# Kernel optimization log

Hardware: AMD Instinct MI355X
Metric: run time of the kernel (lower is better)

## Reference

```python
import jax, jax.numpy as jnp
import numpy as np

NEG_SLOPE = 0.2  # leaky_relu negative slope (alpha)

def _glorot(key, shape):
    fan_in, fan_out = shape[0], shape[-1]
    lim = jnp.sqrt(6.0 / (fan_in + fan_out))
    return jax.random.uniform(key, shape, jnp.float32, -lim, lim)

def setup_inputs() -> dict:
    key = jax.random.key(0)
    ks = jax.random.split(key, 10)
    N, E, F_IN, HID, HEADS, NCLASS = 50000, 800000, 512, 32, 8, 32
    x = jax.random.normal(ks[0], (N, F_IN), jnp.float32)
    edge_index = jax.random.randint(ks[1], (2, E), 0, N, jnp.int64)
    # layer 1: heads=8, out per head = 32, concat -> 256
    W1 = _glorot(ks[2], (F_IN, HEADS * HID))
    att_src1 = _glorot(ks[3], (HEADS, HID))
    att_dst1 = _glorot(ks[4], (HEADS, HID))
    b1 = jnp.zeros((HEADS * HID,), jnp.float32)
    # layer 2: heads=1, out = nclass
    W2 = _glorot(ks[5], (HEADS * HID, NCLASS))
    att_src2 = _glorot(ks[6], (1, NCLASS))
    att_dst2 = _glorot(ks[7], (1, NCLASS))
    b2 = jnp.zeros((NCLASS,), jnp.float32)
    return {"x": x, "edge_index": edge_index, "W1": W1, "att_src1": att_src1,
            "att_dst1": att_dst1, "b1": b1, "W2": W2, "att_src2": att_src2,
            "att_dst2": att_dst2, "b2": b2}

def gat_conv(x, src, dst, W, a_src, a_dst, bias, num_nodes):
    """PyG GATConv (eval mode, self loops already appended to src/dst)."""
    H, C = a_src.shape
    h = (x @ W).reshape(num_nodes, H, C)                 # [N,H,C]
    score_src = jnp.einsum('nhc,hc->nh', h, a_src)       # [N,H]
    score_dst = jnp.einsum('nhc,hc->nh', h, a_dst)       # [N,H]
    e = jax.nn.leaky_relu(score_src[src] + score_dst[dst], NEG_SLOPE)  # [E,H]
    m = jax.ops.segment_max(e, dst, num_segments=num_nodes)           # [N,H]
    w = jnp.exp(e - m[dst])
    denom = jax.ops.segment_sum(w, dst, num_segments=num_nodes)       # [N,H]
    alpha = w / (denom[dst] + 1e-16)                                  # [E,H]
    out = jax.ops.segment_sum(alpha[:, :, None] * h[src], dst,
                              num_segments=num_nodes)                 # [N,H,C]
    return out.reshape(num_nodes, H * C) + bias

def reference(x, edge_index, W1, att_src1, att_dst1, b1, W2, att_src2, att_dst2, b2):
    N = x.shape[0]
    loops = jnp.arange(N, dtype=edge_index.dtype)
    src = jnp.concatenate([edge_index[0], loops])  # PyG add_self_loops=True
    dst = jnp.concatenate([edge_index[1], loops])
    h = jax.nn.elu(gat_conv(x, src, dst, W1, att_src1, att_dst1, b1, N))
    out = gat_conv(h, src, dst, W2, att_src2, att_dst2, b2, N)
    return out + 1e-06
```

## Files before the change

kernel.cpp:

```cpp
#include <hip/hip_runtime.h>
#include <math.h>

#define N_NODES 50000
#define N_EDGES 800000
#define E2 (N_EDGES + N_NODES)
#define F_IN 512
#define HEADS 8
#define HID 32
#define HC 256
#define NCLASS 32
#define NEG_SLOPE 0.2f

typedef unsigned int uint;
typedef unsigned short ushort;
typedef __attribute__((ext_vector_type(8))) short bf16x8;
typedef __attribute__((ext_vector_type(4))) float f32x4;

#define GLOBAL_LOAD_LDS16(g, l) \
    __builtin_amdgcn_global_load_lds((const __attribute__((address_space(1))) void*)(g), \
                                     (__attribute__((address_space(3))) void*)(l), 16, 0, 0)

__device__ inline uint bf16_rne_bits(float f) {
    uint u = __float_as_uint(f);
    return (u + 0x7fffu + ((u >> 16) & 1u)) >> 16;
}
__device__ inline float bf2f(ushort u) { return __uint_as_float(((uint)u) << 16); }

__global__ void split_w1t_kernel(const float* __restrict__ W1,
                                 ushort* __restrict__ hi, ushort* __restrict__ lo) {
    int t = blockIdx.x * 256 + threadIdx.x;
    int n = t >> 9, k = t & 511;
    float f = W1[k * 256 + n];
    uint h = bf16_rne_bits(f);
    float r = f - __uint_as_float(h << 16);
    hi[t] = (ushort)h;
    lo[t] = (ushort)bf16_rne_bits(r);
}

__global__ void split_w2t_kernel(const float* __restrict__ W2,
                                 ushort* __restrict__ hi, ushort* __restrict__ lo) {
    int t = blockIdx.x * 256 + threadIdx.x;
    int n = t >> 8, k = t & 255;
    float f = W2[k * 32 + n];
    uint h = bf16_rne_bits(f);
    float r = f - __uint_as_float(h << 16);
    hi[t] = (ushort)h;
    lo[t] = (ushort)bf16_rne_bits(r);
}

__global__ void __launch_bounds__(256) gemm1_mfma_kernel(const uint* __restrict__ xp,
        const ushort* __restrict__ bhi, const ushort* __restrict__ blo,
        const float* __restrict__ as1, const float* __restrict__ ad1,
        ushort* __restrict__ C, float* __restrict__ ssrc, float* __restrict__ sdst, int M) {
    __shared__ uint   As[128 * 32];
    __shared__ ushort Bh[128 * 32];
    __shared__ ushort Bl[128 * 32];
    const int tid = threadIdx.x, lane = tid & 63, wave = tid >> 6;
    const int bm = blockIdx.x * 128, bn = blockIdx.y * 128;

    const uint* agp[4]; const uint* alp[4];
    #pragma unroll
    for (int s = 0; s < 4; ++s) {
        int t = wave * 4 + s;
        int p = t * 64 + lane;
        int row = p >> 3, cs = p & 7;
        int c = cs ^ (row & 7);
        int grow = bm + row; if (grow > M - 1) grow = M - 1;
        agp[s] = xp + ((size_t)grow * 512 + c * 4);
        alp[s] = &As[t * 256];
    }
    const ushort* bhgp[2]; const ushort* blgp[2]; const ushort* bhlp[2]; const ushort* bllp[2];
    #pragma unroll
    for (int s = 0; s < 2; ++s) {
        int t = wave * 2 + s;
        int p = t * 64 + lane;
        int row = p >> 2, qs = p & 3;
        int q = qs ^ ((row >> 1) & 3);
        size_t go = (size_t)(bn + row) * 512 + q * 8;
        bhgp[s] = bhi + go; blgp[s] = blo + go;
        bhlp[s] = &Bh[t * 512]; bllp[s] = &Bl[t * 512];
    }

    f32x4 acc[4][4] = {};
    const int wm = (wave >> 1) * 64, wn = (wave & 1) * 64;
    const int fm = lane & 15, quad = lane >> 4;

    for (int kk = 0; kk < 16; ++kk) {
        #pragma unroll
        for (int s = 0; s < 4; ++s) GLOBAL_LOAD_LDS16(agp[s], alp[s]);
        #pragma unroll
        for (int s = 0; s < 2; ++s) {
            GLOBAL_LOAD_LDS16(bhgp[s], bhlp[s]);
            GLOBAL_LOAD_LDS16(blgp[s], bllp[s]);
        }
        #pragma unroll
        for (int s = 0; s < 4; ++s) agp[s] += 32;
        #pragma unroll
        for (int s = 0; s < 2; ++s) { bhgp[s] += 32; blgp[s] += 32; }
        __syncthreads();

        bf16x8 ah[4], al[4], bh[4], bl[4];
        #pragma unroll
        for (int i = 0; i < 4; ++i) {
            int row = wm + i * 16 + fm;
            int sw = row & 7;
            uint4 c0 = *(const uint4*)&As[row * 32 + (((2 * quad)     ^ sw) * 4)];
            uint4 c1 = *(const uint4*)&As[row * 32 + (((2 * quad + 1) ^ sw) * 4)];
            union { uint u[4]; bf16x8 v; } H, L;
            H.u[0] = __builtin_amdgcn_perm(c0.y, c0.x, 0x07060302u);
            H.u[1] = __builtin_amdgcn_perm(c0.w, c0.z, 0x07060302u);
            H.u[2] = __builtin_amdgcn_perm(c1.y, c1.x, 0x07060302u);
            H.u[3] = __builtin_amdgcn_perm(c1.w, c1.z, 0x07060302u);
            uint r0 = __float_as_uint(__uint_as_float(c0.x) - __uint_as_float(c0.x & 0xffff0000u));
            uint r1 = __float_as_uint(__uint_as_float(c0.y) - __uint_as_float(c0.y & 0xffff0000u));
            uint r2 = __float_as_uint(__uint_as_float(c0.z) - __uint_as_float(c0.z & 0xffff0000u));
            uint r3 = __float_as_uint(__uint_as_float(c0.w) - __uint_as_float(c0.w & 0xffff0000u));
            uint r4 = __float_as_uint(__uint_as_float(c1.x) - __uint_as_float(c1.x & 0xffff0000u));
            uint r5 = __float_as_uint(__uint_as_float(c1.y) - __uint_as_float(c1.y & 0xffff0000u));
            uint r6 = __float_as_uint(__uint_as_float(c1.z) - __uint_as_float(c1.z & 0xffff0000u));
            uint r7 = __float_as_uint(__uint_as_float(c1.w) - __uint_as_float(c1.w & 0xffff0000u));
            L.u[0] = __builtin_amdgcn_perm(r1, r0, 0x07060302u);
            L.u[1] = __builtin_amdgcn_perm(r3, r2, 0x07060302u);
            L.u[2] = __builtin_amdgcn_perm(r5, r4, 0x07060302u);
            L.u[3] = __builtin_amdgcn_perm(r7, r6, 0x07060302u);
            ah[i] = H.v; al[i] = L.v;
        }
        #pragma unroll
        for (int j = 0; j < 4; ++j) {
            int row = wn + j * 16 + fm;
            int qs = quad ^ ((row >> 1) & 3);
            bh[j] = *(const bf16x8*)&Bh[row * 32 + qs * 8];
            bl[j] = *(const bf16x8*)&Bl[row * 32 + qs * 8];
        }
        #pragma unroll
        for (int i = 0; i < 4; ++i)
            #pragma unroll
            for (int j = 0; j < 4; ++j) {
                acc[i][j] = __builtin_amdgcn_mfma_f32_16x16x32_bf16(ah[i], bh[j], acc[i][j], 0, 0, 0);
                acc[i][j] = __builtin_amdgcn_mfma_f32_16x16x32_bf16(ah[i], bl[j], acc[i][j], 0, 0, 0);
                acc[i][j] = __builtin_amdgcn_mfma_f32_16x16x32_bf16(al[i], bh[j], acc[i][j], 0, 0, 0);
            }
        __syncthreads();
    }

    #pragma unroll
    for (int i = 0; i < 4; ++i) {
        int rb = bm + wm + i * 16 + quad * 4;
        #pragma unroll
        for (int j = 0; j < 4; ++j) {
            int col = bn + wn + j * 16 + fm;
            #pragma unroll
            for (int r = 0; r < 4; ++r) {
                int row = rb + r;
                if (row < M) C[(size_t)row * 256 + col] = (ushort)bf16_rne_bits(acc[i][j][r]);
            }
        }
    }

    const int head0 = (bn + wn) >> 5;
    const float asA0 = as1[head0 * 32 + fm],      asA1 = as1[head0 * 32 + 16 + fm];
    const float asB0 = as1[head0 * 32 + 32 + fm], asB1 = as1[head0 * 32 + 48 + fm];
    const float adA0 = ad1[head0 * 32 + fm],      adA1 = ad1[head0 * 32 + 16 + fm];
    const float adB0 = ad1[head0 * 32 + 32 + fm], adB1 = ad1[head0 * 32 + 48 + fm];
    #pragma unroll
    for (int i = 0; i < 4; ++i) {
        #pragma unroll
        for (int r = 0; r < 4; ++r) {
            int row = bm + wm + i * 16 + quad * 4 + r;
            float s1A = acc[i][0][r] * asA0 + acc[i][1][r] * asA1;
            float s1B = acc[i][2][r] * asB0 + acc[i][3][r] * asB1;
            float s2A = acc[i][0][r] * adA0 + acc[i][1][r] * adA1;
            float s2B = acc[i][2][r] * adB0 + acc[i][3][r] * adB1;
            #pragma unroll
            for (int off = 1; off < 16; off <<= 1) {
                s1A += __shfl_xor(s1A, off);
                s1B += __shfl_xor(s1B, off);
                s2A += __shfl_xor(s2A, off);
                s2B += __shfl_xor(s2B, off);
            }
            if (fm == 0 && row < M) {
                ssrc[(size_t)row * 8 + head0]     = s1A;
                ssrc[(size_t)row * 8 + head0 + 1] = s1B;
                sdst[(size_t)row * 8 + head0]     = s2A;
                sdst[(size_t)row * 8 + head0 + 1] = s2B;
            }
        }
    }
}

__global__ void __launch_bounds__(256) gemm2_mfma_kernel(const ushort* __restrict__ A,
        const ushort* __restrict__ bh_g, const ushort* __restrict__ bl_g,
        const float* __restrict__ as2, const float* __restrict__ ad2,
        ushort* __restrict__ C, float* __restrict__ ssrc, float* __restrict__ sdst, int M) {
    __shared__ ushort As[128 * 32];
    const int tid = threadIdx.x, lane = tid & 63, wave = tid >> 6;
    const int bm = blockIdx.x * 128;
    const int fm = lane & 15, quad = lane >> 4;
    const int wrow = wave * 32;

    const ushort* agp[2]; const ushort* alp[2];
    #pragma unroll
    for (int s = 0; s < 2; ++s) {
        int t = wave * 2 + s;
        int p = t * 64 + lane;
        int row = p >> 2, qs = p & 3;
        int q = qs ^ ((row >> 1) & 3);
        int gr = bm + row; if (gr > M - 1) gr = M - 1;
        agp[s] = A + (size_t)gr * 256 + q * 8;
        alp[s] = &As[t * 512];
    }

    f32x4 acc[2][2] = {};
    for (int kk = 0; kk < 8; ++kk) {
        GLOBAL_LOAD_LDS16(agp[0], alp[0]);
        GLOBAL_LOAD_LDS16(agp[1], alp[1]);
        agp[0] += 32; agp[1] += 32;
        __syncthreads();
        bf16x8 a[2], bh[2], bl[2];
        #pragma unroll
        for (int i = 0; i < 2; ++i) {
            int row = wrow + i * 16 + fm;
            int q = quad ^ ((row >> 1) & 3);
            a[i] = *(const bf16x8*)&As[row * 32 + q * 8];
        }
        #pragma unroll
        for (int j = 0; j < 2; ++j) {
            size_t off = (size_t)(j * 16 + fm) * 256 + kk * 32 + quad * 8;
            bh[j] = *(const bf16x8*)(bh_g + off);
            bl[j] = *(const bf16x8*)(bl_g + off);
        }
        #pragma unroll
        for (int i = 0; i < 2; ++i)
            #pragma unroll
            for (int j = 0; j < 2; ++j) {
                acc[i][j] = __builtin_amdgcn_mfma_f32_16x16x32_bf16(a[i], bh[j], acc[i][j], 0, 0, 0);
                acc[i][j] = __builtin_amdgcn_mfma_f32_16x16x32_bf16(a[i], bl[j], acc[i][j], 0, 0, 0);
            }
        __syncthreads();
    }

    float a0 = as2[fm], a1 = as2[16 + fm];
    float d0 = ad2[fm], d1 = ad2[16 + fm];
    #pragma unroll
    for (int i = 0; i < 2; ++i) {
        #pragma unroll
        for (int r = 0; r < 4; ++r) {
            int rg = bm + wrow + i * 16 + quad * 4 + r;
            float v0 = acc[i][0][r], v1 = acc[i][1][r];
            float s1 = v0 * a0 + v1 * a1;
            float s2 = v0 * d0 + v1 * d1;
            #pragma unroll
            for (int off = 1; off < 16; off <<= 1) {
                s1 += __shfl_xor(s1, off);
                s2 += __shfl_xor(s2, off);
            }
            if (rg < M) {
                C[(size_t)rg * 32 + fm]      = (ushort)bf16_rne_bits(v0);
                C[(size_t)rg * 32 + 16 + fm] = (ushort)bf16_rne_bits(v1);
                if (fm == 0) { ssrc[rg] = s1; sdst[rg] = s2; }
            }
        }
    }
}

__global__ void count_deg(const int* __restrict__ ei, int* __restrict__ deg) {
    int e = blockIdx.x * blockDim.x + threadIdx.x;
    if (e >= E2) return;
    int dst = (e < N_EDGES) ? ei[N_EDGES + e] : (e - N_EDGES);
    atomicAdd(&deg[dst], 1);
}

#define SCAN_B 256
#define SCAN_NB ((N_NODES + SCAN_B - 1) / SCAN_B)

__global__ void scan1_kernel(const int* __restrict__ deg, int* __restrict__ rowstart,
                             int* __restrict__ blocksum) {
    __shared__ int sm[SCAN_B];
    int t = threadIdx.x, i = blockIdx.x * SCAN_B + t;
    int v = (i < N_NODES) ? deg[i] : 0;
    sm[t] = v; __syncthreads();
    int x = v;
    for (int off = 1; off < SCAN_B; off <<= 1) {
        int y = (t >= off) ? sm[t - off] : 0; __syncthreads();
        x += y; sm[t] = x; __syncthreads();
    }
    if (i <= N_NODES) rowstart[i] = x - v;
    if (t == SCAN_B - 1) blocksum[blockIdx.x] = x;
}

__global__ void scan2_kernel(const int* __restrict__ blocksum, int* __restrict__ blockoff) {
    __shared__ int sm[256];
    int t = threadIdx.x;
    int v = (t < SCAN_NB) ? blocksum[t] : 0;
    sm[t] = v; __syncthreads();
    int x = v;
    for (int off = 1; off < 256; off <<= 1) {
        int y = (t >= off) ? sm[t - off] : 0; __syncthreads();
        x += y; sm[t] = x; __syncthreads();
    }
    if (t < SCAN_NB) blockoff[t] = x - v;
}

__global__ void fill_csr(const int* __restrict__ ei, const int* __restrict__ rowstart,
                         const int* __restrict__ blockoff,
                         int* __restrict__ cursor, int* __restrict__ csr_src) {
    int e = blockIdx.x * blockDim.x + threadIdx.x;
    if (e >= E2) return;
    int src, dst;
    if (e < N_EDGES) { src = ei[e]; dst = ei[N_EDGES + e]; }
    else             { src = e - N_EDGES; dst = src; }
    int p = atomicAdd(&cursor[dst], 1);
    csr_src[rowstart[dst] + blockoff[dst >> 8] + p] = src;
}

__global__ void __launch_bounds__(256) agg1_wave_kernel(const ushort* __restrict__ h,
        const float* __restrict__ ssrc, const float* __restrict__ sdst,
        const int* __restrict__ rowstart, const int* __restrict__ blockoff,
        const int* __restrict__ csr_src,
        const float* __restrict__ bias, ushort* __restrict__ out) {
    const int wid = (blockIdx.x * blockDim.x + threadIdx.x) >> 6;
    if (wid >= N_NODES) return;
    const int lane = threadIdx.x & 63;
    const int hg = lane >> 3;
    const int hl = lane & 7;
    const int n = wid;
    const int beg = rowstart[n] + blockoff[n >> 8];
    const int end = rowstart[n + 1] + blockoff[(n + 1) >> 8];
    const float sdst_n = sdst[(size_t)n * HEADS + hg];

    float4 acc = make_float4(0.f, 0.f, 0.f, 0.f);
    float sw = 0.f;
    const ushort* hc = h + lane * 4;
    const int base = hg << 3;
    for (int e = beg; e < end; e += 16) {
        int ee0 = e + hl, ee1 = e + 8 + hl;
        int ei0 = ee0 < end ? ee0 : end - 1;
        int ei1 = ee1 < end ? ee1 : end - 1;
        int s0 = csr_src[ei0];
        int s1 = csr_src[ei1];
        float c0 = ssrc[(size_t)s0 * HEADS + hg] + sdst_n;
        float c1 = ssrc[(size_t)s1 * HEADS + hg] + sdst_n;
        c0 = c0 > 0.f ? c0 : NEG_SLOPE * c0;
        c1 = c1 > 0.f ? c1 : NEG_SLOPE * c1;
        float w0 = (ee0 < end) ? __expf(c0) : 0.f;
        float w1 = (ee1 < end) ? __expf(c1) : 0.f;
        float wj[16]; int sj[16];
        #pragma unroll
        for (int j = 0; j < 8; ++j) {
            wj[j]     = __shfl(w0, base + j);
            sj[j]     = __shfl(s0, base + j);
            wj[8 + j] = __shfl(w1, base + j);
            sj[8 + j] = __shfl(s1, base + j);
        }
        ushort4 v[16];
        #pragma unroll
        for (int j = 0; j < 16; ++j) v[j] = *(const ushort4*)(hc + (size_t)sj[j] * HC);
        #pragma unroll
        for (int j = 0; j < 16; ++j) {
            acc.x += wj[j] * bf2f(v[j].x);
            acc.y += wj[j] * bf2f(v[j].y);
            acc.z += wj[j] * bf2f(v[j].z);
            acc.w += wj[j] * bf2f(v[j].w);
            sw += wj[j];
        }
    }
    float inv = 1.f / (sw + 1e-16f);
    float4 bv = *(const float4*)(bias + lane * 4);
    float4 o;
    o.x = acc.x * inv + bv.x; o.y = acc.y * inv + bv.y;
    o.z = acc.z * inv + bv.z; o.w = acc.w * inv + bv.w;
    o.x = o.x > 0.f ? o.x : expm1f(o.x);
    o.y = o.y > 0.f ? o.y : expm1f(o.y);
    o.z = o.z > 0.f ? o.z : expm1f(o.z);
    o.w = o.w > 0.f ? o.w : expm1f(o.w);
    ushort4 ob;
    ob.x = (ushort)bf16_rne_bits(o.x);
    ob.y = (ushort)bf16_rne_bits(o.y);
    ob.z = (ushort)bf16_rne_bits(o.z);
    ob.w = (ushort)bf16_rne_bits(o.w);
    *(ushort4*)(out + (size_t)n * HC + lane * 4) = ob;
}

__global__ void __launch_bounds__(256) agg2_kernel(const ushort* __restrict__ h2,
        const float* __restrict__ ssrc, const float* __restrict__ sdst,
        const int* __restrict__ rowstart, const int* __restrict__ blockoff,
        const int* __restrict__ csr_src,
        const float* __restrict__ bias, float* __restrict__ out) {
    const int n = blockIdx.x * 4 + (threadIdx.x >> 6);
    if (n >= N_NODES) return;
    const int beg = rowstart[n] + blockoff[n >> 8];
    const int end = rowstart[n + 1] + blockoff[(n + 1) >> 8];
    const int t = threadIdx.x & 63;
    const float sdst_n = sdst[n];

    const int slot = t >> 4, cp = t & 15;
    float a0 = 0.f, a1 = 0.f, sw = 0.f;
    for (int e = beg + slot; e < end; e += 4) {
        int src = csr_src[e];
        float sc = ssrc[src] + sdst_n;
        sc = sc > 0.f ? sc : NEG_SLOPE * sc;
        float w = __expf(sc);
        uint v = *(const uint*)(h2 + (size_t)src * NCLASS + cp * 2);
        a0 += w * __uint_as_float(v << 16);
        a1 += w * __uint_as_float(v & 0xffff0000u);
        sw += w;
    }
    a0 += __shfl_down(a0, 32); a1 += __shfl_down(a1, 32); sw += __shfl_down(sw, 32);
    a0 += __shfl_down(a0, 16); a1 += __shfl_down(a1, 16); sw += __shfl_down(sw, 16);
    if (t < 16) {
        float inv = 1.f / (sw + 1e-16f);
        float2 o;
        o.x = a0 * inv + bias[cp * 2]     + 1e-6f;
        o.y = a1 * inv + bias[cp * 2 + 1] + 1e-6f;
        *(float2*)(out + (size_t)n * NCLASS + cp * 2) = o;
    }
}

extern "C" void kernel_launch(void* const* d_in, const int* in_sizes, int n_in,
                              void* d_out, int out_size, void* d_ws, size_t ws_size,
                              hipStream_t stream) {
    const float* x        = (const float*)d_in[0];
    const int*   ei       = (const int*)  d_in[1];
    const float* W1       = (const float*)d_in[2];
    const float* att_src1 = (const float*)d_in[3];
    const float* att_dst1 = (const float*)d_in[4];
    const float* b1       = (const float*)d_in[5];
    const float* W2       = (const float*)d_in[6];
    const float* att_src2 = (const float*)d_in[7];
    const float* att_dst2 = (const float*)d_in[8];
    const float* b2       = (const float*)d_in[9];
    float* out = (float*)d_out;

    ushort* w1t_hi = (ushort*)d_ws;
    ushort* w1t_lo = w1t_hi + 256 * 512;
    ushort* w2t_hi = w1t_lo + 256 * 512;
    ushort* w2t_lo = w2t_hi + 32 * 256;
    ushort* h1b    = w2t_lo + 32 * 256;
    ushort* h2b    = h1b + (size_t)N_NODES * HC;
    ushort* out1b  = h2b + (size_t)N_NODES * NCLASS;
    float* ssrc1 = (float*)(out1b + (size_t)N_NODES * HC);
    float* sdst1 = ssrc1 + (size_t)N_NODES * HEADS;
    float* ssrc2 = sdst1 + (size_t)N_NODES * HEADS;
    float* sdst2 = ssrc2 + N_NODES;
    int* rowstart = (int*)(sdst2 + N_NODES);
    int* deg      = rowstart + N_NODES + 1;
    int* cursor   = deg + N_NODES;
    int* csr_src  = cursor + N_NODES;
    int* blocksum = csr_src + E2;
    int* blockoff = blocksum + SCAN_NB;

    hipMemsetAsync(deg, 0, 2 * N_NODES * sizeof(int), stream);
    int eb = (E2 + 255) / 256;
    count_deg<<<eb, 256, 0, stream>>>(ei, deg);
    scan1_kernel<<<SCAN_NB, SCAN_B, 0, stream>>>(deg, rowstart, blocksum);
    scan2_kernel<<<1, 256, 0, stream>>>(blocksum, blockoff);
    fill_csr<<<eb, 256, 0, stream>>>(ei, rowstart, blockoff, cursor, csr_src);

    split_w1t_kernel<<<(256 * 512) / 256, 256, 0, stream>>>(W1, w1t_hi, w1t_lo);
    split_w2t_kernel<<<(32 * 256) / 256, 256, 0, stream>>>(W2, w2t_hi, w2t_lo);

    {
        dim3 grid((N_NODES + 127) / 128, HC / 128);
        gemm1_mfma_kernel<<<grid, 256, 0, stream>>>((const uint*)x, w1t_hi, w1t_lo,
                att_src1, att_dst1, h1b, ssrc1, sdst1, N_NODES);
    }
    agg1_wave_kernel<<<(N_NODES + 3) / 4, 256, 0, stream>>>(h1b, ssrc1, sdst1, rowstart, blockoff, csr_src, b1, out1b);

    gemm2_mfma_kernel<<<(N_NODES + 127) / 128, 256, 0, stream>>>(out1b, w2t_hi, w2t_lo,
            att_src2, att_dst2, h2b, ssrc2, sdst2, N_NODES);
    agg2_kernel<<<(N_NODES + 3) / 4, 256, 0, stream>>>(h2b, ssrc2, sdst2, rowstart, blockoff, csr_src, b2, out);
}
```

Baseline: 410.2 us.

## Load GEMM A operands directly to registers and fuse prep kernels

Merges the W1/W2 bf16 hi/lo split kernels and the degree-count kernel into one launch. In gemm1 the fp32 A tile is now read straight from global memory into registers in MFMA fragment layout instead of being staged through swizzled LDS. In gemm2 the A operand is likewise read directly from global memory and the per-iteration barriers are dropped. This aims to cut launch overhead, LDS traffic and synchronisation, at the cost of less coalesced global reads and the loss of LDS staging for A.

```diff
diff --git a/kernel.cpp b/kernel.cpp
--- a/kernel.cpp
+++ b/kernel.cpp
@@ -26,49 +26,51 @@
 }
 __device__ inline float bf2f(ushort u) { return __uint_as_float(((uint)u) << 16); }
 
-__global__ void split_w1t_kernel(const float* __restrict__ W1,
-                                 ushort* __restrict__ hi, ushort* __restrict__ lo) {
-    int t = blockIdx.x * 256 + threadIdx.x;
-    int n = t >> 9, k = t & 511;
-    float f = W1[k * 256 + n];
-    uint h = bf16_rne_bits(f);
-    float r = f - __uint_as_float(h << 16);
-    hi[t] = (ushort)h;
-    lo[t] = (ushort)bf16_rne_bits(r);
-}
-
-__global__ void split_w2t_kernel(const float* __restrict__ W2,
-                                 ushort* __restrict__ hi, ushort* __restrict__ lo) {
-    int t = blockIdx.x * 256 + threadIdx.x;
-    int n = t >> 8, k = t & 255;
-    float f = W2[k * 32 + n];
-    uint h = bf16_rne_bits(f);
-    float r = f - __uint_as_float(h << 16);
-    hi[t] = (ushort)h;
-    lo[t] = (ushort)bf16_rne_bits(r);
+#define W1_BLOCKS 512
+#define W2_BLOCKS 32
+#define DEG_BLOCKS ((E2 + 255) / 256)
+
+__global__ void __launch_bounds__(256) prep_kernel(const float* __restrict__ W1,
+        ushort* __restrict__ w1hi, ushort* __restrict__ w1lo,
+        const float* __restrict__ W2, ushort* __restrict__ w2hi, ushort* __restrict__ w2lo,
+        const int* __restrict__ ei, int* __restrict__ deg) {
+    int b = blockIdx.x;
+    if (b < W1_BLOCKS) {
+        int t = b * 256 + threadIdx.x;
+        int n = t >> 9, k = t & 511;
+        float f = W1[k * 256 + n];
+        uint h = bf16_rne_bits(f);
+        float r = f - __uint_as_float(h << 16);
+        w1hi[t] = (ushort)h;
+        w1lo[t] = (ushort)bf16_rne_bits(r);
+    } else if (b < W1_BLOCKS + W2_BLOCKS) {
+        int t = (b - W1_BLOCKS) * 256 + threadIdx.x;
+        int n = t >> 8, k = t & 255;
+        float f = W2[k * 32 + n];
+        uint h = bf16_rne_bits(f);
+        float r = f - __uint_as_float(h << 16);
+        w2hi[t] = (ushort)h;
+        w2lo[t] = (ushort)bf16_rne_bits(r);
+    } else {
+        int e = (b - W1_BLOCKS - W2_BLOCKS) * 256 + threadIdx.x;
+        if (e < E2) {
+            int dst = (e < N_EDGES) ? ei[N_EDGES + e] : (e - N_EDGES);
+            atomicAdd(&deg[dst], 1);
+        }
+    }
 }
 
 __global__ void __launch_bounds__(256) gemm1_mfma_kernel(const uint* __restrict__ xp,
         const ushort* __restrict__ bhi, const ushort* __restrict__ blo,
         const float* __restrict__ as1, const float* __restrict__ ad1,
         ushort* __restrict__ C, float* __restrict__ ssrc, float* __restrict__ sdst, int M) {
-    __shared__ uint   As[128 * 32];
     __shared__ ushort Bh[128 * 32];
     __shared__ ushort Bl[128 * 32];
     const int tid = threadIdx.x, lane = tid & 63, wave = tid >> 6;
     const int bm = blockIdx.x * 128, bn = blockIdx.y * 128;
-
-    const uint* agp[4]; const uint* alp[4];
-    #pragma unroll
-    for (int s = 0; s < 4; ++s) {
-        int t = wave * 4 + s;
-        int p = t * 64 + lane;
-        int row = p >> 3, cs = p & 7;
-        int c = cs ^ (row & 7);
-        int grow = bm + row; if (grow > M - 1) grow = M - 1;
-        agp[s] = xp + ((size_t)grow * 512 + c * 4);
-        alp[s] = &As[t * 256];
-    }
+    const int wm = (wave >> 1) * 64, wn = (wave & 1) * 64;
+    const int fm = lane & 15, quad = lane >> 4;
+
     const ushort* bhgp[2]; const ushort* blgp[2]; const ushort* bhlp[2]; const ushort* bllp[2];
     #pragma unroll
     for (int s = 0; s < 2; ++s) {
@@ -81,31 +83,35 @@
         bhlp[s] = &Bh[t * 512]; bllp[s] = &Bl[t * 512];
     }
 
+    const uint* ap[4];
+    #pragma unroll
+    for (int i = 0; i < 4; ++i) {
+        int gr = bm + wm + i * 16 + fm; if (gr > M - 1) gr = M - 1;
+        ap[i] = xp + (size_t)gr * 512 + quad * 8;
+    }
+
     f32x4 acc[4][4] = {};
-    const int wm = (wave >> 1) * 64, wn = (wave & 1) * 64;
-    const int fm = lane & 15, quad = lane >> 4;
 
     for (int kk = 0; kk < 16; ++kk) {
-        #pragma unroll
-        for (int s = 0; s < 4; ++s) GLOBAL_LOAD_LDS16(agp[s], alp[s]);
         #pragma unroll
         for (int s = 0; s < 2; ++s) {
             GLOBAL_LOAD_LDS16(bhgp[s], bhlp[s]);
             GLOBAL_LOAD_LDS16(blgp[s], bllp[s]);
-        }
-        #pragma unroll
-        for (int s = 0; s < 4; ++s) agp[s] += 32;
-        #pragma unroll
-        for (int s = 0; s < 2; ++s) { bhgp[s] += 32; blgp[s] += 32; }
+            bhgp[s] += 32; blgp[s] += 32;
+        }
+        uint4 ar0[4], ar1[4];
+        #pragma unroll
+        for (int i = 0; i < 4; ++i) {
+            ar0[i] = *(const uint4*)ap[i];
+            ar1[i] = *(const uint4*)(ap[i] + 4);
+            ap[i] += 32;
+        }
         __syncthreads();
 
         bf16x8 ah[4], al[4], bh[4], bl[4];
         #pragma unroll
         for (int i = 0; i < 4; ++i) {
-            int row = wm + i * 16 + fm;
-            int sw = row & 7;
-            uint4 c0 = *(const uint4*)&As[row * 32 + (((2 * quad)     ^ sw) * 4)];
-            uint4 c1 = *(const uint4*)&As[row * 32 + (((2 * quad + 1) ^ sw) * 4)];
+            uint4 c0 = ar0[i], c1 = ar1[i];
             union { uint u[4]; bf16x8 v; } H, L;
             H.u[0] = __builtin_amdgcn_perm(c0.y, c0.x, 0x07060302u);
             H.u[1] = __builtin_amdgcn_perm(c0.w, c0.z, 0x07060302u);
@@ -192,37 +198,24 @@
         const ushort* __restrict__ bh_g, const ushort* __restrict__ bl_g,
         const float* __restrict__ as2, const float* __restrict__ ad2,
         ushort* __restrict__ C, float* __restrict__ ssrc, float* __restrict__ sdst, int M) {
-    __shared__ ushort As[128 * 32];
     const int tid = threadIdx.x, lane = tid & 63, wave = tid >> 6;
     const int bm = blockIdx.x * 128;
     const int fm = lane & 15, quad = lane >> 4;
     const int wrow = wave * 32;
 
-    const ushort* agp[2]; const ushort* alp[2];
-    #pragma unroll
-    for (int s = 0; s < 2; ++s) {
-        int t = wave * 2 + s;
-        int p = t * 64 + lane;
-        int row = p >> 2, qs = p & 3;
-        int q = qs ^ ((row >> 1) & 3);
-        int gr = bm + row; if (gr > M - 1) gr = M - 1;
-        agp[s] = A + (size_t)gr * 256 + q * 8;
-        alp[s] = &As[t * 512];
+    int gr[2];
+    #pragma unroll
+    for (int i = 0; i < 2; ++i) {
+        gr[i] = bm + wrow + i * 16 + fm;
+        if (gr[i] > M - 1) gr[i] = M - 1;
     }
 
     f32x4 acc[2][2] = {};
     for (int kk = 0; kk < 8; ++kk) {
-        GLOBAL_LOAD_LDS16(agp[0], alp[0]);
-        GLOBAL_LOAD_LDS16(agp[1], alp[1]);
-        agp[0] += 32; agp[1] += 32;
-        __syncthreads();
         bf16x8 a[2], bh[2], bl[2];
         #pragma unroll
-        for (int i = 0; i < 2; ++i) {
-            int row = wrow + i * 16 + fm;
-            int q = quad ^ ((row >> 1) & 3);
-            a[i] = *(const bf16x8*)&As[row * 32 + q * 8];
-        }
+        for (int i = 0; i < 2; ++i)
+            a[i] = *(const bf16x8*)(A + (size_t)gr[i] * 256 + kk * 32 + quad * 8);
         #pragma unroll
         for (int j = 0; j < 2; ++j) {
             size_t off = (size_t)(j * 16 + fm) * 256 + kk * 32 + quad * 8;
@@ -236,7 +229,6 @@
                 acc[i][j] = __builtin_amdgcn_mfma_f32_16x16x32_bf16(a[i], bh[j], acc[i][j], 0, 0, 0);
                 acc[i][j] = __builtin_amdgcn_mfma_f32_16x16x32_bf16(a[i], bl[j], acc[i][j], 0, 0, 0);
             }
-        __syncthreads();
     }
 
     float a0 = as2[fm], a1 = as2[16 + fm];
@@ -261,13 +253,6 @@
             }
         }
     }
-}
-
-__global__ void count_deg(const int* __restrict__ ei, int* __restrict__ deg) {
-    int e = blockIdx.x * blockDim.x + threadIdx.x;
-    if (e >= E2) return;
-    int dst = (e < N_EDGES) ? ei[N_EDGES + e] : (e - N_EDGES);
-    atomicAdd(&deg[dst], 1);
 }
 
 #define SCAN_B 256
@@ -450,14 +435,12 @@
     int* blockoff = blocksum + SCAN_NB;
 
     hipMemsetAsync(deg, 0, 2 * N_NODES * sizeof(int), stream);
-    int eb = (E2 + 255) / 256;
-    count_deg<<<eb, 256, 0, stream>>>(ei, deg);
+    prep_kernel<<<W1_BLOCKS + W2_BLOCKS + DEG_BLOCKS, 256, 0, stream>>>(
+            W1, w1t_hi, w1t_lo, W2, w2t_hi, w2t_lo, ei, deg);
     scan1_kernel<<<SCAN_NB, SCAN_B, 0, stream>>>(deg, rowstart, blocksum);
     scan2_kernel<<<1, 256, 0, stream>>>(blocksum, blockoff);
+    int eb = (E2 + 255) / 256;
     fill_csr<<<eb, 256, 0, stream>>>(ei, rowstart, blockoff, cursor, csr_src);
-
-    split_w1t_kernel<<<(256 * 512) / 256, 256, 0, stream>>>(W1, w1t_hi, w1t_lo);
-    split_w2t_kernel<<<(32 * 256) / 256, 256, 0, stream>>>(W2, w2t_hi, w2t_lo);
 
     {
         dim3 grid((N_NODES + 127) / 128, HC / 128);
```

New measurement: 431.6 us. 1.05x slower.
